# Performance work log

Hardware: AMD Instinct MI355X
Metric: run time of the kernel (lower is better)

## Reference

```python
import jax, jax.numpy as jnp
import numpy as np


def setup_inputs() -> dict:
    key = jax.random.key(0)
    k1, k2, k3, k4, k5 = jax.random.split(key, 5)
    B, C, G, H, W = 2, 64, 4, 64, 64
    CG = C * G            # 256 complex input channels (flattened)
    DQK = max(C // 8, 1)  # 8  query/key channels after gabor pooling
    scale = 1.0 / np.sqrt(CG)
    x = jax.random.normal(k1, (2, B, C, G, H, W), dtype=jnp.float32)
    wq = jax.random.normal(k2, (2, DQK, CG), dtype=jnp.float32) * scale
    wk = jax.random.normal(k3, (2, DQK, CG), dtype=jnp.float32) * scale
    wv = jax.random.normal(k4, (2, CG, CG), dtype=jnp.float32) * scale
    gamma = jax.random.normal(k5, (1,), dtype=jnp.float32) * 0.1
    return {"x": x, "wq": wq, "wk": wk, "wv": wv, "gamma": gamma}


def _cconv1x1(w, xr, xi):
    """Complex 1x1 conv: (wr+i wi)(xr+i xi). w: (2,O,Cin), x: (B,Cin,L)."""
    wr, wi = w[0], w[1]
    yr = jnp.einsum('oc,bcl->bol', wr, xr) - jnp.einsum('oc,bcl->bol', wi, xi)
    yi = jnp.einsum('oc,bcl->bol', wr, xi) + jnp.einsum('oc,bcl->bol', wi, xr)
    return yr, yi


def reference(x, wq, wk, wv, gamma):
    _, B, C, G, H, W = x.shape
    L = H * W
    xr = x[0].reshape(B, C * G, L)
    xi = x[1].reshape(B, C * G, L)
    # complex Q (B,d,L) / K (B,d,L)
    qr, qi = _cconv1x1(wq, xr, xi)
    kr, ki = _cconv1x1(wk, xr, xi)
    # energy = Q^H-free complex bmm: energy[b,l,m] = sum_d q[b,d,l] * k[b,d,m]
    er = jnp.einsum('bdl,bdm->blm', qr, kr) - jnp.einsum('bdl,bdm->blm', qi, ki)
    ei = jnp.einsum('bdl,bdm->blm', qr, ki) + jnp.einsum('bdl,bdm->blm', qi, kr)
    # magnitude-squared softmax over last axis -> real attention (B,L,L)
    att = jax.nn.softmax(er * er + ei * ei, axis=-1)
    # complex V (B,CG,L); out[b,c,m] = sum_l v[b,c,l] * att[b,m,l]
    vr, vi = _cconv1x1(wv, xr, xi)
    out_r = jnp.einsum('bcl,bml->bcm', vr, att)
    out_i = jnp.einsum('bcl,bml->bcm', vi, att)
    out = jnp.stack([out_r, out_i]).reshape(2, B, C, G, H, W)
    return gamma * out + x
```

## Files before the change

### kernel.cpp

```cpp
#include <hip/hip_runtime.h>
#include <cstdint>

constexpr int Bc  = 2;
constexpr int CGc = 256;
constexpr int Dc  = 8;
constexpr int Lc  = 4096;

typedef __attribute__((ext_vector_type(8))) short short8;
typedef __attribute__((ext_vector_type(4))) float floatx4;

__device__ inline unsigned short f2bf(float f) {
  union { float f; unsigned u; } v; v.f = f;
  unsigned r = v.u + 0x7fffu + ((v.u >> 16) & 1u);
  return (unsigned short)(r >> 16);
}
__device__ inline float bf2f(unsigned short h) {
  return __uint_as_float((unsigned)h << 16);
}

__global__ __launch_bounds__(256) void prep_pack(const float* __restrict__ x,
                                                 const float* __restrict__ wv,
                                                 unsigned short* __restrict__ Xlk,
                                                 unsigned short* __restrict__ Wcat) {
  const int tid = threadIdx.x;
  const int z   = blockIdx.z;
  if (z >= 2) {
    const int i  = ((((z - 2) * 8 + blockIdx.y) * 64 + blockIdx.x) << 8) + tid;
    const int cc = i >> 9, k = i & 511;
    const int co = cc >> 8, c = cc & 255, ci = k >> 8, cin = k & 255;
    const float wr = wv[(size_t)c * CGc + cin];
    const float wi = wv[(size_t)(CGc + c) * CGc + cin];
    const float val = co == 0 ? (ci == 0 ? wr : -wi) : (ci == 0 ? wi : wr);
    Wcat[i] = f2bf(val);
    return;
  }
  __shared__ float xs[64][65];
  const int b   = z;
  const int l0  = blockIdx.x * 64;
  const int c0  = blockIdx.y * 64;
  const int lt  = tid & 63, r4 = tid >> 6;
#pragma unroll
  for (int p = 0; p < 16; ++p) {
    const int row  = p * 4 + r4;
    const int cin2 = c0 + row;
    const int comp = cin2 >> 8, cin = cin2 & 255;
    xs[row][lt] = x[((size_t)(comp * Bc + b) * CGc + cin) * Lc + l0 + lt];
  }
  __syncthreads();
#pragma unroll
  for (int p = 0; p < 16; ++p) {
    const int lr = p * 4 + r4;
    Xlk[((size_t)b * Lc + l0 + lr) * 512 + c0 + lt] = f2bf(xs[lt][lr]);
  }
}

__global__ __launch_bounds__(1024, 4) void qk_projpack(const float* __restrict__ x,
                                                       const float* __restrict__ wq,
                                                       const float* __restrict__ wk,
                                                       unsigned short* __restrict__ Qcat,
                                                       unsigned short* __restrict__ K1hi,
                                                       unsigned short* __restrict__ K1lo,
                                                       unsigned short* __restrict__ K2hi,
                                                       unsigned short* __restrict__ K2lo) {
  __shared__ float ws[4 * Dc * CGc];
  __shared__ float pq[4][32][17];
  __shared__ float pk[4][32][17];
  const int tid = threadIdx.x;
  const int b   = blockIdx.y;
  for (int i = tid; i < 2 * Dc * CGc; i += 1024) {
    ws[i]                 = wq[i];
    ws[2 * Dc * CGc + i]  = wk[i];
  }
  __syncthreads();
  const int cg  = tid >> 8;
  const int sub = tid & 255;
  const int d   = sub >> 5;
  const int ml  = sub & 31;
  const int m   = blockIdx.x * 32 + ml;
  const int c0  = cg * 64;
  const float* xr = x + ((size_t)(0 * Bc + b) * CGc + c0) * Lc + m;
  const float* xi = x + ((size_t)(1 * Bc + b) * CGc + c0) * Lc + m;
  const float* wqr = ws + d * CGc + c0;
  const float* wqi = ws + (Dc + d) * CGc + c0;
  const float* wkr = ws + 2 * Dc * CGc + d * CGc + c0;
  const float* wki = ws + 2 * Dc * CGc + (Dc + d) * CGc + c0;
  float qer = 0.f, qei = 0.f, ker = 0.f, kei = 0.f;
#pragma unroll 4
  for (int cin = 0; cin < 64; ++cin) {
    const float vr = xr[(size_t)cin * Lc];
    const float vi = xi[(size_t)cin * Lc];
    const float a1 = wqr[cin], b1 = wqi[cin];
    qer = fmaf(a1, vr, qer); qer = fmaf(-b1, vi, qer);
    qei = fmaf(a1, vi, qei); qei = fmaf(b1, vr, qei);
    const float a2 = wkr[cin], b2 = wki[cin];
    ker = fmaf(a2, vr, ker); ker = fmaf(-b2, vi, ker);
    kei = fmaf(a2, vi, kei); kei = fmaf(b2, vr, kei);
  }
  pq[cg][ml][d]     = qer;
  pq[cg][ml][8 + d] = qei;
  pk[cg][ml][d]     = ker;
  pk[cg][ml][8 + d] = kei;
  __syncthreads();
  if (tid < 256) {
    const int part = tid >> 5;
    const int rl   = tid & 31;
    const size_t r = (size_t)b * Lc + blockIdx.x * 32 + rl;
    if (part < 2) {
      unsigned u[8];
#pragma unroll
      for (int t = 0; t < 8; ++t) {
        const float v0 = ((pq[0][rl][2 * t] + pq[1][rl][2 * t]) + pq[2][rl][2 * t]) + pq[3][rl][2 * t];
        const float v1 = ((pq[0][rl][2 * t + 1] + pq[1][rl][2 * t + 1]) + pq[2][rl][2 * t + 1]) + pq[3][rl][2 * t + 1];
        const unsigned short h0 = f2bf(v0), h1 = f2bf(v1);
        if (part == 0) {
          u[t] = (unsigned)h0 | ((unsigned)h1 << 16);
        } else {
          const unsigned short l0 = f2bf(v0 - bf2f(h0));
          const unsigned short l1 = f2bf(v1 - bf2f(h1));
          u[t] = (unsigned)l0 | ((unsigned)l1 << 16);
        }
      }
      uint4* dst = (uint4*)(Qcat + r * 32 + part * 16);
      dst[0] = make_uint4(u[0], u[1], u[2], u[3]);
      dst[1] = make_uint4(u[4], u[5], u[6], u[7]);
    } else if (part < 6) {
      float ksum[16];
#pragma unroll
      for (int e = 0; e < 16; ++e)
        ksum[e] = ((pk[0][rl][e] + pk[1][rl][e]) + pk[2][rl][e]) + pk[3][rl][e];
      float kv[16];
      if (part < 4) {
#pragma unroll
        for (int e = 0; e < 8; ++e) { kv[e] = ksum[e]; kv[8 + e] = -ksum[8 + e]; }
      } else {
#pragma unroll
        for (int e = 0; e < 8; ++e) { kv[e] = ksum[8 + e]; kv[8 + e] = ksum[e]; }
      }
      const int lo = part & 1;
      unsigned u[8];
#pragma unroll
      for (int t = 0; t < 8; ++t) {
        const unsigned short h0 = f2bf(kv[2 * t]), h1 = f2bf(kv[2 * t + 1]);
        if (!lo) {
          u[t] = (unsigned)h0 | ((unsigned)h1 << 16);
        } else {
          const unsigned short l0 = f2bf(kv[2 * t] - bf2f(h0));
          const unsigned short l1 = f2bf(kv[2 * t + 1] - bf2f(h1));
          u[t] = (unsigned)l0 | ((unsigned)l1 << 16);
        }
      }
      unsigned short* base = part < 4 ? (lo ? K1lo : K1hi) : (lo ? K2lo : K2hi);
      uint4* dst = (uint4*)(base + r * 16);
      dst[0] = make_uint4(u[0], u[1], u[2], u[3]);
      dst[1] = make_uint4(u[4], u[5], u[6], u[7]);
    }
  }
}

__global__ __launch_bounds__(256) void v_gemm(const unsigned short* __restrict__ Wcat,
                                              const unsigned short* __restrict__ Xlk,
                                              unsigned short* __restrict__ vbf) {
  __shared__ short As[128 * 64];
  __shared__ short Bs[64 * 64];
  const int tid  = threadIdx.x;
  const int b    = blockIdx.z;
  const int cc0  = blockIdx.x * 128;
  const int l0   = blockIdx.y * 64;
  const int wid  = tid >> 6, lane = tid & 63;
  const int wcc  = (wid >> 1) * 64;
  const int wl   = (wid & 1) * 32;
  const int lrow = lane & 15, quad = lane >> 4;
  floatx4 acc[4][2] = {};
  const unsigned short* wsrc = Wcat + (size_t)cc0 * 512;
  const unsigned short* xsrc = Xlk + ((size_t)b * Lc + l0) * 512;
  int s_off[4], g_off[4];
#pragma unroll
  for (int r = 0; r < 4; ++r) {
    const int idx = r * 256 + tid;
    const int row = idx >> 3, ch = idx & 7;
    s_off[r] = row * 64 + (ch ^ (row & 7)) * 8;
    g_off[r] = row * 512 + ch * 8;
  }
  short8 ar[4], br[2];
#pragma unroll
  for (int r = 0; r < 4; ++r) ar[r] = *(const short8*)(wsrc + g_off[r]);
#pragma unroll
  for (int r = 0; r < 2; ++r) br[r] = *(const short8*)(xsrc + g_off[r]);
  for (int k0 = 0; k0 < 512; k0 += 64) {
    __syncthreads();
#pragma unroll
    for (int r = 0; r < 4; ++r) *(short8*)&As[s_off[r]] = ar[r];
#pragma unroll
    for (int r = 0; r < 2; ++r) *(short8*)&Bs[s_off[r]] = br[r];
    __syncthreads();
    if (k0 + 64 < 512) {
#pragma unroll
      for (int r = 0; r < 4; ++r) ar[r] = *(const short8*)(wsrc + g_off[r] + k0 + 64);
#pragma unroll
      for (int r = 0; r < 2; ++r) br[r] = *(const short8*)(xsrc + g_off[r] + k0 + 64);
    }
#pragma unroll
    for (int kk = 0; kk < 64; kk += 32) {
      const int cb = kk >> 3;
      short8 af[4], bf[2];
#pragma unroll
      for (int i = 0; i < 4; ++i)
        af[i] = *(const short8*)&As[(wcc + i * 16 + lrow) * 64 +
                                    ((cb + quad) ^ (lrow & 7)) * 8];
#pragma unroll
      for (int j = 0; j < 2; ++j)
        bf[j] = *(const short8*)&Bs[(wl + j * 16 + lrow) * 64 +
                                    ((cb + quad) ^ (lrow & 7)) * 8];
#pragma unroll
      for (int i = 0; i < 4; ++i)
#pragma unroll
        for (int j = 0; j < 2; ++j)
          acc[i][j] = __builtin_amdgcn_mfma_f32_16x16x32_bf16(af[i], bf[j], acc[i][j], 0, 0, 0);
    }
  }
#pragma unroll
  for (int i = 0; i < 4; ++i) {
    const int ccb = cc0 + wcc + i * 16 + quad * 4;
#pragma unroll
    for (int j = 0; j < 2; ++j) {
      const int l = l0 + wl + j * 16 + lrow;
#pragma unroll
      for (int rg = 0; rg < 4; ++rg)
        vbf[((size_t)b * 512 + ccb + rg) * Lc + l] = f2bf(acc[i][j][rg]);
    }
  }
}

__global__ __launch_bounds__(1024, 8) void emax_exp(const unsigned short* __restrict__ Qcat,
                                                    const unsigned short* __restrict__ K1hi,
                                                    const unsigned short* __restrict__ K1lo,
                                                    const unsigned short* __restrict__ K2hi,
                                                    const unsigned short* __restrict__ K2lo,
                                                    unsigned short* __restrict__ att,
                                                    float* __restrict__ Ssum) {
  __shared__ unsigned maxb[16];
  __shared__ float    sumb[16];
  const int tid  = threadIdx.x;
  const int wid  = tid >> 6, lane = tid & 63;
  const int lrow = lane & 15, quad = lane >> 4, qsel = quad & 1;
  const int b    = blockIdx.y;
  const int m16  = blockIdx.x * 16;
  const int lbeg = wid * 256;
  const size_t kb = (size_t)b * Lc;
  if (tid < 16) { maxb[tid] = 0u; sumb[tid] = 0.f; }
  __syncthreads();
  const short8 afrag = *(const short8*)(Qcat + (kb + m16 + lrow) * 32 + quad * 8);
  float mx[4] = {0.f, 0.f, 0.f, 0.f};
  for (int l0 = lbeg; l0 < lbeg + 256; l0 += 32) {
    short8 b1h[2], b2h[2];
#pragma unroll
    for (int u = 0; u < 2; ++u) {
      const size_t l = kb + l0 + u * 16 + lrow;
      b1h[u] = *(const short8*)(K1hi + l * 16 + qsel * 8);
      b2h[u] = *(const short8*)(K2hi + l * 16 + qsel * 8);
    }
#pragma unroll
    for (int u = 0; u < 2; ++u) {
      const floatx4 er = __builtin_amdgcn_mfma_f32_16x16x32_bf16(afrag, b1h[u], (floatx4){0.f, 0.f, 0.f, 0.f}, 0, 0, 0);
      const floatx4 ei = __builtin_amdgcn_mfma_f32_16x16x32_bf16(afrag, b2h[u], (floatx4){0.f, 0.f, 0.f, 0.f}, 0, 0, 0);
#pragma unroll
      for (int r = 0; r < 4; ++r) {
        float e = er[r] * er[r];
        e = fmaf(ei[r], ei[r], e);
        mx[r] = fmaxf(mx[r], e);
      }
    }
  }
#pragma unroll
  for (int r = 0; r < 4; ++r) {
    float v = mx[r];
#pragma unroll
    for (int off = 1; off < 16; off <<= 1) v = fmaxf(v, __shfl_xor(v, off));
    if (lrow == 0)
      atomicMax(&maxb[quad * 4 + r], __float_as_uint(v));
  }
  __syncthreads();
  float Mv[4], sum[4] = {};
#pragma unroll
  for (int r = 0; r < 4; ++r) Mv[r] = __uint_as_float(maxb[quad * 4 + r]);
  for (int l0 = lbeg; l0 < lbeg + 256; l0 += 32) {
    short8 b1h[2], b1l[2], b2h[2], b2l[2];
#pragma unroll
    for (int u = 0; u < 2; ++u) {
      const size_t l = kb + l0 + u * 16 + lrow;
      b1h[u] = *(const short8*)(K1hi + l * 16 + qsel * 8);
      b1l[u] = *(const short8*)(K1lo + l * 16 + qsel * 8);
      b2h[u] = *(const short8*)(K2hi + l * 16 + qsel * 8);
      b2l[u] = *(const short8*)(K2lo + l * 16 + qsel * 8);
    }
#pragma unroll
    for (int u = 0; u < 2; ++u) {
      floatx4 er = __builtin_amdgcn_mfma_f32_16x16x32_bf16(afrag, b1l[u], (floatx4){0.f, 0.f, 0.f, 0.f}, 0, 0, 0);
      er = __builtin_amdgcn_mfma_f32_16x16x32_bf16(afrag, b1h[u], er, 0, 0, 0);
      floatx4 ei = __builtin_amdgcn_mfma_f32_16x16x32_bf16(afrag, b2l[u], (floatx4){0.f, 0.f, 0.f, 0.f}, 0, 0, 0);
      ei = __builtin_amdgcn_mfma_f32_16x16x32_bf16(afrag, b2h[u], ei, 0, 0, 0);
#pragma unroll
      for (int r = 0; r < 4; ++r) {
        float e = er[r] * er[r];
        e = fmaf(ei[r], ei[r], e);
        const float wgt = __expf(e - Mv[r]);
        sum[r] += wgt;
        att[(kb + m16 + quad * 4 + r) * Lc + l0 + u * 16 + lrow] = f2bf(wgt);
      }
    }
  }
#pragma unroll
  for (int r = 0; r < 4; ++r) {
    float v = sum[r];
#pragma unroll
    for (int off = 1; off < 16; off <<= 1) v += __shfl_xor(v, off);
    if (lrow == 0) atomicAdd(&sumb[quad * 4 + r], v);
  }
  __syncthreads();
  if (tid < 16) Ssum[kb + m16 + tid] = sumb[tid];
}

__device__ __forceinline__ void pv_stage128(const unsigned short* __restrict__ vsrc,
                                            const unsigned short* __restrict__ asrc,
                                            short* lds_buf, int k0, int wid, int lane) {
  const int rsub = lane >> 4;
  const int cs   = lane & 15;
#pragma unroll
  for (int t = 0; t < 4; ++t) {
    const int q    = wid * 4 + t;
    const int tile = q >> 5;
    const int j    = q & 31;
    const int row  = j * 4 + rsub;
    const int gch  = cs ^ (row & 7);
    const unsigned short* g =
        (tile == 0 ? vsrc : asrc) + (size_t)row * Lc + k0 + gch * 8;
    short* l = lds_buf + tile * 16384 + j * 512;
    __builtin_amdgcn_global_load_lds(
        (const __attribute__((address_space(1))) void*)g,
        (__attribute__((address_space(3))) void*)l, 16, 0, 0);
  }
}

__device__ __forceinline__ void pv_compute128(const short* __restrict__ As,
                                              const short* __restrict__ Bs,
                                              int cb, int wcc, int wm, int lrow, int quad,
                                              floatx4 (&acc)[4][4]) {
  short8 af[4], bf[4];
#pragma unroll
  for (int i = 0; i < 4; ++i)
    af[i] = *(const short8*)&As[(wcc + i * 16 + lrow) * 128 +
                                ((cb + quad) ^ (lrow & 7)) * 8];
#pragma unroll
  for (int j = 0; j < 4; ++j)
    bf[j] = *(const short8*)&Bs[(wm + j * 16 + lrow) * 128 +
                                ((cb + quad) ^ (lrow & 7)) * 8];
  __builtin_amdgcn_s_setprio(1);
#pragma unroll
  for (int i = 0; i < 4; ++i)
#pragma unroll
    for (int j = 0; j < 4; ++j)
      acc[i][j] = __builtin_amdgcn_mfma_f32_16x16x32_bf16(af[i], bf[j], acc[i][j], 0, 0, 0);
  __builtin_amdgcn_s_setprio(0);
}

__global__ __launch_bounds__(1024, 1) void pv_gemm(const unsigned short* __restrict__ v,
                                                   const unsigned short* __restrict__ att,
                                                   const float* __restrict__ Ssum,
                                                   const float* __restrict__ x,
                                                   const float* __restrict__ gamma,
                                                   float* __restrict__ out) {
  extern __shared__ short smem[];
  const int flat = blockIdx.x;
  const int swz  = (flat & 7) * 32 + (flat >> 3);
  const int b    = swz >> 7;
  const int rem  = swz & 127;
  const int m0   = (rem >> 2) * 128;
  const int cc0  = (rem & 3) * 128;
  const int tid  = threadIdx.x;
  const int wid  = tid >> 6, lane = tid & 63;
  const int g    = wid >> 2;
  const int w4   = wid & 3;
  const int wcc  = (w4 >> 1) * 64;
  const int wm   = (w4 & 1) * 64;
  const int lrow = lane & 15, quad = lane >> 4;
  const int cb   = g * 4;
  floatx4 acc[4][4] = {};
  const unsigned short* vsrc = v   + ((size_t)b * 512 + cc0) * Lc;
  const unsigned short* asrc = att + ((size_t)b * Lc + m0) * Lc;
  pv_stage128(vsrc, asrc, smem, 0, wid, lane);
  for (int p = 0; p < 32; ++p) {
    asm volatile("s_waitcnt vmcnt(0)" ::: "memory");
    __builtin_amdgcn_s_barrier();
    __builtin_amdgcn_sched_barrier(0);
    if (p + 1 < 32)
      pv_stage128(vsrc, asrc, smem + ((p + 1) & 1) * 32768, (p + 1) * 128, wid, lane);
    pv_compute128(smem + (p & 1) * 32768, smem + (p & 1) * 32768 + 16384,
                  cb, wcc, wm, lrow, quad, acc);
    __builtin_amdgcn_sched_barrier(0);
  }
  __syncthreads();
  float* red = (float*)smem;
  if (g == 1 || g == 3) {
    float* dst = red + (g == 3 ? 16384 : 0);
#pragma unroll
    for (int i = 0; i < 4; ++i)
#pragma unroll
      for (int j = 0; j < 4; ++j) {
        const int tq = i * 4 + j;
        *(floatx4*)&dst[(tq * 256 + w4 * 64 + lane) * 4] = acc[i][j];
      }
  }
  __syncthreads();
  if (g == 0 || g == 2) {
    const float* src = red + (g == 2 ? 16384 : 0);
#pragma unroll
    for (int i = 0; i < 4; ++i)
#pragma unroll
      for (int j = 0; j < 4; ++j) {
        const int tq = i * 4 + j;
        const floatx4 o = *(const floatx4*)&src[(tq * 256 + w4 * 64 + lane) * 4];
        acc[i][j] += o;
      }
  }
  __syncthreads();
  if (g == 2) {
#pragma unroll
    for (int i = 0; i < 4; ++i)
#pragma unroll
      for (int j = 0; j < 4; ++j) {
        const int tq = i * 4 + j;
        *(floatx4*)&red[(tq * 256 + w4 * 64 + lane) * 4] = acc[i][j];
      }
  }
  __syncthreads();
  if (g == 0) {
#pragma unroll
    for (int i = 0; i < 4; ++i)
#pragma unroll
      for (int j = 0; j < 4; ++j) {
        const int tq = i * 4 + j;
        const floatx4 o = *(const floatx4*)&red[(tq * 256 + w4 * 64 + lane) * 4];
        acc[i][j] += o;
      }
    const float gm = gamma[0];
    float svj[4];
#pragma unroll
    for (int j = 0; j < 4; ++j)
      svj[j] = gm / Ssum[(size_t)b * Lc + m0 + wm + j * 16 + lrow];
#pragma unroll
    for (int i = 0; i < 4; ++i) {
      const int ccb = cc0 + wcc + i * 16 + quad * 4;
#pragma unroll
      for (int j = 0; j < 4; ++j) {
        const int m = m0 + wm + j * 16 + lrow;
#pragma unroll
        for (int rg = 0; rg < 4; ++rg) {
          const int cc   = ccb + rg;
          const int comp = cc >> 8, c = cc & 255;
          const size_t idx = (((size_t)comp * Bc + b) * CGc + c) * Lc + m;
          out[idx] = svj[j] * acc[i][j][rg] + x[idx];
        }
      }
    }
  }
}

extern "C" void kernel_launch(void* const* d_in, const int* in_sizes, int n_in,
                              void* d_out, int out_size, void* d_ws, size_t ws_size,
                              hipStream_t stream) {
  const float* x     = (const float*)d_in[0];
  const float* wq    = (const float*)d_in[1];
  const float* wk    = (const float*)d_in[2];
  const float* wv    = (const float*)d_in[3];
  const float* gamma = (const float*)d_in[4];
  float* out = (float*)d_out;

  float* q    = (float*)d_ws;
  float* kk   = q    + (size_t)Bc * Lc * 16;
  float* Mrow = kk   + (size_t)Bc * Lc * 16;
  float* Ssum = Mrow + (size_t)Bc * Lc;
  unsigned short* vbf  = (unsigned short*)(Ssum + (size_t)Bc * Lc);
  unsigned short* att  = vbf + (size_t)Bc * 512 * Lc;
  unsigned short* Xlk  = att;
  unsigned short* Qcat = att + (size_t)Bc * Lc * Lc;
  unsigned short* K1hi = Qcat + (size_t)Bc * Lc * 32;
  unsigned short* K1lo = K1hi + (size_t)Bc * Lc * 16;
  unsigned short* K2hi = K1lo + (size_t)Bc * Lc * 16;
  unsigned short* K2lo = K2hi + (size_t)Bc * Lc * 16;
  unsigned short* Wcat = K2lo + (size_t)Bc * Lc * 16;

  prep_pack<<<dim3(64, 8, 4), 256, 0, stream>>>(x, wv, Xlk, Wcat);
  qk_projpack<<<dim3(Lc / 32, Bc), 1024, 0, stream>>>(x, wq, wk, Qcat, K1hi, K1lo, K2hi, K2lo);
  v_gemm<<<dim3(512 / 128, Lc / 64, Bc), 256, 0, stream>>>(Wcat, Xlk, vbf);
  emax_exp<<<dim3(Lc / 16, Bc), 1024, 0, stream>>>(Qcat, K1hi, K1lo, K2hi, K2lo, att, Ssum);
  pv_gemm<<<dim3(256), 1024, 2 * 32768 * sizeof(short), stream>>>(vbf, att, Ssum, x, gamma, out);
}
```

Measured before the change: 168.2 us.

## Restructure V GEMM with async LDS double buffering and split-K warp groups

The V projection GEMM now uses 1024-thread blocks on 128x128 tiles. Each K=128 slab is streamed straight into double-buffered shared memory with global_load_lds, and the slab's K range is split across four wave groups, whose partial accumulators are then reduced through LDS. It also raises MFMA issue priority during compute. The aim is to overlap global loads with MFMA work and drop the register round trip. The cost is a multi-step LDS reduction with extra barriers and half as many blocks in the grid.

```diff
diff --git a/kernel.cpp b/kernel.cpp
--- a/kernel.cpp
+++ b/kernel.cpp
@@ -157,76 +157,132 @@
   }
 }
 
-__global__ __launch_bounds__(256) void v_gemm(const unsigned short* __restrict__ Wcat,
-                                              const unsigned short* __restrict__ Xlk,
-                                              unsigned short* __restrict__ vbf) {
-  __shared__ short As[128 * 64];
-  __shared__ short Bs[64 * 64];
-  const int tid  = threadIdx.x;
+__device__ __forceinline__ void vg_stage128(const unsigned short* __restrict__ asrc_w,
+                                            const unsigned short* __restrict__ bsrc_x,
+                                            short* lds_buf, int k0, int wid, int lane) {
+  const int rsub = lane >> 4;
+  const int cs   = lane & 15;
+#pragma unroll
+  for (int t = 0; t < 4; ++t) {
+    const int q    = wid * 4 + t;
+    const int tile = q >> 5;
+    const int j    = q & 31;
+    const int row  = j * 4 + rsub;
+    const int gch  = cs ^ (row & 7);
+    const unsigned short* g =
+        (tile == 0 ? asrc_w : bsrc_x) + (size_t)row * 512 + k0 + gch * 8;
+    short* l = lds_buf + tile * 16384 + j * 512;
+    __builtin_amdgcn_global_load_lds(
+        (const __attribute__((address_space(1))) void*)g,
+        (__attribute__((address_space(3))) void*)l, 16, 0, 0);
+  }
+}
+
+__device__ __forceinline__ void vg_compute128(const short* __restrict__ As,
+                                              const short* __restrict__ Bs,
+                                              int cb, int wcc, int wm, int lrow, int quad,
+                                              floatx4 (&acc)[4][4]) {
+  short8 af[4], bf[4];
+#pragma unroll
+  for (int i = 0; i < 4; ++i)
+    af[i] = *(const short8*)&As[(wcc + i * 16 + lrow) * 128 +
+                                ((cb + quad) ^ (lrow & 7)) * 8];
+#pragma unroll
+  for (int j = 0; j < 4; ++j)
+    bf[j] = *(const short8*)&Bs[(wm + j * 16 + lrow) * 128 +
+                                ((cb + quad) ^ (lrow & 7)) * 8];
+  __builtin_amdgcn_s_setprio(1);
+#pragma unroll
+  for (int i = 0; i < 4; ++i)
+#pragma unroll
+    for (int j = 0; j < 4; ++j)
+      acc[i][j] = __builtin_amdgcn_mfma_f32_16x16x32_bf16(af[i], bf[j], acc[i][j], 0, 0, 0);
+  __builtin_amdgcn_s_setprio(0);
+}
+
+__global__ __launch_bounds__(1024, 1) void v_gemm(const unsigned short* __restrict__ Wcat,
+                                                  const unsigned short* __restrict__ Xlk,
+                                                  unsigned short* __restrict__ vbf) {
+  extern __shared__ short smem[];
   const int b    = blockIdx.z;
   const int cc0  = blockIdx.x * 128;
-  const int l0   = blockIdx.y * 64;
+  const int l0   = blockIdx.y * 128;
+  const int tid  = threadIdx.x;
   const int wid  = tid >> 6, lane = tid & 63;
-  const int wcc  = (wid >> 1) * 64;
-  const int wl   = (wid & 1) * 32;
+  const int g    = wid >> 2;
+  const int w4   = wid & 3;
+  const int wcc  = (w4 >> 1) * 64;
+  const int wm   = (w4 & 1) * 64;
   const int lrow = lane & 15, quad = lane >> 4;
-  floatx4 acc[4][2] = {};
-  const unsigned short* wsrc = Wcat + (size_t)cc0 * 512;
-  const unsigned short* xsrc = Xlk + ((size_t)b * Lc + l0) * 512;
-  int s_off[4], g_off[4];
-#pragma unroll
-  for (int r = 0; r < 4; ++r) {
-    const int idx = r * 256 + tid;
-    const int row = idx >> 3, ch = idx & 7;
-    s_off[r] = row * 64 + (ch ^ (row & 7)) * 8;
-    g_off[r] = row * 512 + ch * 8;
-  }
-  short8 ar[4], br[2];
-#pragma unroll
-  for (int r = 0; r < 4; ++r) ar[r] = *(const short8*)(wsrc + g_off[r]);
-#pragma unroll
-  for (int r = 0; r < 2; ++r) br[r] = *(const short8*)(xsrc + g_off[r]);
-  for (int k0 = 0; k0 < 512; k0 += 64) {
-    __syncthreads();
-#pragma unroll
-    for (int r = 0; r < 4; ++r) *(short8*)&As[s_off[r]] = ar[r];
-#pragma unroll
-    for (int r = 0; r < 2; ++r) *(short8*)&Bs[s_off[r]] = br[r];
-    __syncthreads();
-    if (k0 + 64 < 512) {
-#pragma unroll
-      for (int r = 0; r < 4; ++r) ar[r] = *(const short8*)(wsrc + g_off[r] + k0 + 64);
-#pragma unroll
-      for (int r = 0; r < 2; ++r) br[r] = *(const short8*)(xsrc + g_off[r] + k0 + 64);
-    }
-#pragma unroll
-    for (int kk = 0; kk < 64; kk += 32) {
-      const int cb = kk >> 3;
-      short8 af[4], bf[2];
-#pragma unroll
-      for (int i = 0; i < 4; ++i)
-        af[i] = *(const short8*)&As[(wcc + i * 16 + lrow) * 64 +
-                                    ((cb + quad) ^ (lrow & 7)) * 8];
-#pragma unroll
-      for (int j = 0; j < 2; ++j)
-        bf[j] = *(const short8*)&Bs[(wl + j * 16 + lrow) * 64 +
-                                    ((cb + quad) ^ (lrow & 7)) * 8];
-#pragma unroll
-      for (int i = 0; i < 4; ++i)
-#pragma unroll
-        for (int j = 0; j < 2; ++j)
-          acc[i][j] = __builtin_amdgcn_mfma_f32_16x16x32_bf16(af[i], bf[j], acc[i][j], 0, 0, 0);
-    }
-  }
-#pragma unroll
-  for (int i = 0; i < 4; ++i) {
-    const int ccb = cc0 + wcc + i * 16 + quad * 4;
-#pragma unroll
-    for (int j = 0; j < 2; ++j) {
-      const int l = l0 + wl + j * 16 + lrow;
-#pragma unroll
-      for (int rg = 0; rg < 4; ++rg)
-        vbf[((size_t)b * 512 + ccb + rg) * Lc + l] = f2bf(acc[i][j][rg]);
+  const int cb   = g * 4;
+  floatx4 acc[4][4] = {};
+  const unsigned short* asrc_w = Wcat + (size_t)cc0 * 512;
+  const unsigned short* bsrc_x = Xlk + ((size_t)b * Lc + l0) * 512;
+  vg_stage128(asrc_w, bsrc_x, smem, 0, wid, lane);
+  for (int p = 0; p < 4; ++p) {
+    asm volatile("s_waitcnt vmcnt(0)" ::: "memory");
+    __builtin_amdgcn_s_barrier();
+    __builtin_amdgcn_sched_barrier(0);
+    if (p + 1 < 4)
+      vg_stage128(asrc_w, bsrc_x, smem + ((p + 1) & 1) * 32768, (p + 1) * 128, wid, lane);
+    vg_compute128(smem + (p & 1) * 32768, smem + (p & 1) * 32768 + 16384,
+                  cb, wcc, wm, lrow, quad, acc);
+    __builtin_amdgcn_sched_barrier(0);
+  }
+  __syncthreads();
+  float* red = (float*)smem;
+  if (g == 1 || g == 3) {
+    float* dst = red + (g == 3 ? 16384 : 0);
+#pragma unroll
+    for (int i = 0; i < 4; ++i)
+#pragma unroll
+      for (int j = 0; j < 4; ++j) {
+        const int tq = i * 4 + j;
+        *(floatx4*)&dst[(tq * 256 + w4 * 64 + lane) * 4] = acc[i][j];
+      }
+  }
+  __syncthreads();
+  if (g == 0 || g == 2) {
+    const float* src = red + (g == 2 ? 16384 : 0);
+#pragma unroll
+    for (int i = 0; i < 4; ++i)
+#pragma unroll
+      for (int j = 0; j < 4; ++j) {
+        const int tq = i * 4 + j;
+        const floatx4 o = *(const floatx4*)&src[(tq * 256 + w4 * 64 + lane) * 4];
+        acc[i][j] += o;
+      }
+  }
+  __syncthreads();
+  if (g == 2) {
+#pragma unroll
+    for (int i = 0; i < 4; ++i)
+#pragma unroll
+      for (int j = 0; j < 4; ++j) {
+        const int tq = i * 4 + j;
+        *(floatx4*)&red[(tq * 256 + w4 * 64 + lane) * 4] = acc[i][j];
+      }
+  }
+  __syncthreads();
+  if (g == 0) {
+#pragma unroll
+    for (int i = 0; i < 4; ++i)
+#pragma unroll
+      for (int j = 0; j < 4; ++j) {
+        const int tq = i * 4 + j;
+        const floatx4 o = *(const floatx4*)&red[(tq * 256 + w4 * 64 + lane) * 4];
+        acc[i][j] += o;
+      }
+#pragma unroll
+    for (int i = 0; i < 4; ++i) {
+      const int ccb = cc0 + wcc + i * 16 + quad * 4;
+#pragma unroll
+      for (int j = 0; j < 4; ++j) {
+        const int l = l0 + wm + j * 16 + lrow;
+#pragma unroll
+        for (int rg = 0; rg < 4; ++rg)
+          vbf[((size_t)b * 512 + ccb + rg) * Lc + l] = f2bf(acc[i][j][rg]);
+      }
     }
   }
 }
@@ -491,7 +547,7 @@
 
   prep_pack<<<dim3(64, 8, 4), 256, 0, stream>>>(x, wv, Xlk, Wcat);
   qk_projpack<<<dim3(Lc / 32, Bc), 1024, 0, stream>>>(x, wq, wk, Qcat, K1hi, K1lo, K2hi, K2lo);
-  v_gemm<<<dim3(512 / 128, Lc / 64, Bc), 256, 0, stream>>>(Wcat, Xlk, vbf);
+  v_gemm<<<dim3(512 / 128, Lc / 128, Bc), 1024, 2 * 32768 * sizeof(short), stream>>>(Wcat, Xlk, vbf);
   emax_exp<<<dim3(Lc / 16, Bc), 1024, 0, stream>>>(Qcat, K1hi, K1lo, K2hi, K2lo, att, Ssum);
   pv_gemm<<<dim3(256), 1024, 2 * 32768 * sizeof(short), stream>>>(vbf, att, Ssum, x, gamma, out);
 }
```

Measured after the change: 169.2 us (median of 2 runs). No clear change (+0.6%).
